# Kernel tuning notes

Measured on AMD Instinct MI355X. Metric: run time of the kernel, lower is better.

The kernel has to match this reference:

```python
import jax, jax.numpy as jnp
import numpy as np

THRESHOLD = 0.9  # graph_threshold; graph_secondary is None
EPS = 1e-12


def setup_inputs() -> dict:
    key = jax.random.key(0)
    k_x, k_cw, k_cb, k_u, k_lw, k_lb = jax.random.split(key, 6)
    B = 8192
    x = jax.random.normal(k_x, (B, 1, 28, 28), dtype=jnp.float32)
    conv_w = jax.random.normal(k_cw, (4, 1, 2, 2), dtype=jnp.float32) * 0.5  # OIHW
    conv_b = jax.random.normal(k_cb, (4,), dtype=jnp.float32) * 0.1
    # random orthogonal 4x4 "quantum" unitary via QR, as in the torch buffer
    unitary = jnp.linalg.qr(jax.random.normal(k_u, (4, 4), dtype=jnp.float32))[0]
    D = 4 * 14 * 14  # conv_out * num_patches = 784
    lin_w = jax.random.normal(k_lw, (10, D), dtype=jnp.float32) * (1.0 / np.sqrt(D))
    lin_b = jax.random.normal(k_lb, (10,), dtype=jnp.float32) * 0.01
    return {"x": x, "conv_w": conv_w, "conv_b": conv_b, "unitary": unitary,
            "lin_w": lin_w, "lin_b": lin_b}


def _forward(x, conv_w, conv_b, unitary, lin_w, lin_b):
    B = x.shape[0]
    # _PatchConv: 2x2 conv, stride 2, then flatten to [B, 4*14*14]
    feats = jax.lax.conv_general_dilated(
        x, conv_w, window_strides=(2, 2), padding="VALID",
        dimension_numbers=("NCHW", "OIHW", "NCHW"))
    feats = feats + conv_b[None, :, None, None]
    flat = feats.reshape(B, -1)                      # [B, 784]
    # _QuantumPatchEncoder: reinterpret as [B, 196, 4], apply unitary^T
    patches = flat.reshape(B, -1, 4)
    qf = jnp.einsum("bnk,wk->bnw", patches, unitary).reshape(B, -1)  # [B, 784]
    # linear head + log_softmax
    logits = qf @ lin_w.T + lin_b
    log_probs = jax.nn.log_softmax(logits, axis=-1)
    # GraphAdjacencyLayer: pairwise squared-cosine fidelity, thresholded.
    # Vectorized: normalize rows, one GEMM, square, threshold.
    qn = qf / (jnp.linalg.norm(qf, axis=-1, keepdims=True) + EPS)   # [B, 784]
    fid = (qn @ qn.T) ** 2                                          # [B, B]
    adj = jnp.where(fid >= THRESHOLD, 1.0, 0.0).astype(jnp.float32)
    adj = adj * (1.0 - jnp.eye(B, dtype=jnp.float32))  # no self-edges (i<j pairs)
    return log_probs, adj


def reference(x, conv_w, conv_b, unitary, lin_w, lin_b):
    return _forward(x, conv_w, conv_b, unitary, lin_w, lin_b)
```

## Files before the change

### kernel.cpp

```cpp
#include <hip/hip_runtime.h>
#include <hip/hip_bf16.h>

typedef unsigned char uchar_t;
typedef __attribute__((ext_vector_type(4))) float f32x4;

#define B_SZ 8192
#define D_FT 784
#define N_KT 13
#define PLANE_U32 131072
#define PLANE_B   524288
#define THRESH 0.9f

#define GLOBAL_AS(p) ((const __attribute__((address_space(1))) void*)(p))
#define LDS_AS(p)    ((__attribute__((address_space(3))) void*)(p))

__global__ __launch_bounds__(256) void preproc_kernel(
    const float* __restrict__ x, const float* __restrict__ conv_w,
    const float* __restrict__ conv_b, const float* __restrict__ unitary,
    const float* __restrict__ lin_w, const float* __restrict__ lin_b,
    float* __restrict__ log_probs, uchar_t* __restrict__ qn)
{
    __shared__ float xr[4][784];
    __shared__ float qf[4][784];

    const int t = threadIdx.x, lane = t & 63, wave = t >> 6;
    const int b = blockIdx.x * 4 + wave;
    float* xw = xr[wave];
    float* qw = qf[wave];

    const float4* xsrc = (const float4*)(x + (size_t)b * 784);
    #pragma unroll
    for (int i = lane; i < 196; i += 64) ((float4*)xw)[i] = xsrc[i];
    __syncthreads();

    float sumsq = 0.f;
    for (int g = lane; g < 196; g += 64) {
        const int c = g / 49, p = g % 49;
        const float w00 = conv_w[c*4+0], w01 = conv_w[c*4+1];
        const float w10 = conv_w[c*4+2], w11 = conv_w[c*4+3];
        const float bcv = conv_b[c];
        float feat[4];
        #pragma unroll
        for (int j = 0; j < 4; ++j) {
            const int s = 4*p + j;
            const int h = s / 14, wq = s % 14;
            const float* px = &xw[(2*h)*28 + 2*wq];
            feat[j] = bcv + w00*px[0] + w01*px[1] + w10*px[28] + w11*px[29];
        }
        #pragma unroll
        for (int w = 0; w < 4; ++w) {
            float v = unitary[w*4+0]*feat[0] + unitary[w*4+1]*feat[1]
                    + unitary[w*4+2]*feat[2] + unitary[w*4+3]*feat[3];
            qw[4*g + w] = v;
            sumsq += v * v;
        }
    }
    __syncthreads();

    #pragma unroll
    for (int off = 1; off < 64; off <<= 1) sumsq += __shfl_xor(sumsq, off, 64);
    const float inv = 1.0f / (sqrtf(sumsq) + 1e-12f);

    unsigned int* qbase = (unsigned int*)qn;
    for (int i = lane; i < 208; i += 64) {
        unsigned int o = 0u;
        if (i < 196) {
            const float v0 = qw[4*i+0] * inv, v1 = qw[4*i+1] * inv;
            const float v2 = qw[4*i+2] * inv, v3 = qw[4*i+3] * inv;
            int lo = __builtin_amdgcn_cvt_pk_fp8_f32(v0, v1, 0, 0);
            o = (unsigned int)__builtin_amdgcn_cvt_pk_fp8_f32(v2, v3, lo, 1);
        }
        qbase[(size_t)(i >> 4) * PLANE_U32 + (size_t)b * 16 + (i & 15)] = o;
    }

    float acc[10];
    #pragma unroll
    for (int cl = 0; cl < 10; ++cl) acc[cl] = 0.f;
    for (int k = lane; k < 784; k += 64) {
        const float v = qw[k];
        #pragma unroll
        for (int cl = 0; cl < 10; ++cl) acc[cl] += v * lin_w[cl*784 + k];
    }
    #pragma unroll
    for (int cl = 0; cl < 10; ++cl) {
        #pragma unroll
        for (int off = 1; off < 64; off <<= 1)
            acc[cl] += __shfl_xor(acc[cl], off, 64);
        acc[cl] += lin_b[cl];
    }
    if (lane == 0) {
        float mx = -1e30f;
        #pragma unroll
        for (int cl = 0; cl < 10; ++cl) mx = fmaxf(mx, acc[cl]);
        float se = 0.f;
        #pragma unroll
        for (int cl = 0; cl < 10; ++cl) se += expf(acc[cl] - mx);
        const float lse = mx + logf(se);
        #pragma unroll
        for (int cl = 0; cl < 10; ++cl)
            log_probs[(size_t)b*10 + cl] = acc[cl] - lse;
    }
}

__global__ __launch_bounds__(256, 4) void gram_kernel(
    const uchar_t* __restrict__ qn, float* __restrict__ adj)
{
    const int t0 = blockIdx.x;
    int tl = (t0 & 7) * 260 + (t0 >> 3);
    int br = (int)((129.0 - sqrt(16641.0 - 8.0 * (double)tl)) * 0.5);
    while ((br + 1) * (129 - (br + 1)) / 2 <= tl) ++br;
    while (br * (129 - br) / 2 > tl) --br;
    const int bc = br + (tl - br * (129 - br) / 2);

    __shared__ uchar_t ldsA[2][8192] __attribute__((aligned(16)));
    __shared__ uchar_t ldsB[2][8192] __attribute__((aligned(16)));

    const int t = threadIdx.x;
    const int lane = t & 63, wave = t >> 6;
    const int wr = wave >> 1, wc = wave & 1;
    const int quad = lane >> 4, l16 = lane & 15;

    const bool offdiag = (br != bc);
    const int br128 = br * 128, bc128 = bc * 128;
    const int zmask = offdiag ? 8191 : 4095;

    const int srow = lane & 15, sck = (lane >> 4) * 16;
    const uchar_t* gA0 = qn + (size_t)(br128 + wave*16     + srow) * 64 + sck;
    const uchar_t* gA1 = qn + (size_t)(br128 + (wave+4)*16 + srow) * 64 + sck;
    const uchar_t* gB0 = qn + (size_t)(bc128 + wave*16     + srow) * 64 + sck;
    const uchar_t* gB1 = qn + (size_t)(bc128 + (wave+4)*16 + srow) * 64 + sck;
    const int ld0 = wave * 1024, ld1 = (wave + 4) * 1024;

    #define STAGE(p, koff) do {                                                            \
        __builtin_amdgcn_global_load_lds(GLOBAL_AS(gA0 + (koff)), LDS_AS(&ldsA[p][ld0]), 16, 0, 0); \
        __builtin_amdgcn_global_load_lds(GLOBAL_AS(gA1 + (koff)), LDS_AS(&ldsA[p][ld1]), 16, 0, 0); \
        __builtin_amdgcn_global_load_lds(GLOBAL_AS(gB0 + (koff)), LDS_AS(&ldsB[p][ld0]), 16, 0, 0); \
        __builtin_amdgcn_global_load_lds(GLOBAL_AS(gB1 + (koff)), LDS_AS(&ldsB[p][ld1]), 16, 0, 0); \
    } while (0)

    f32x4 acc[4][4] = {};
    STAGE(0, 0);

    #pragma unroll
    for (int kt = 0; kt < N_KT; ++kt) {
        const int p = kt & 1;

        asm volatile("" ::: "memory");
        if (kt == 0)
            __builtin_amdgcn_s_waitcnt(0xF70);
        else
            __builtin_amdgcn_s_waitcnt(0xF73);
        __builtin_amdgcn_s_barrier();
        asm volatile("" ::: "memory");

        if (kt + 1 < N_KT) STAGE(p ^ 1, (size_t)(kt + 1) * PLANE_B);
        asm volatile("" ::: "memory");

        {
            f32x4 z = {0.f, 0.f, 0.f, 0.f};
            #pragma unroll
            for (int j = 0; j < 3; ++j) {
                const int idx  = (kt * 768 + j * 256 + t) & zmask;
                const int tile = idx >> 12;
                const int r    = (idx >> 5) & 127;
                const int c4   = idx & 31;
                const int rowb = tile ? bc128 : br128;
                const int colb = tile ? br128 : bc128;
                __builtin_nontemporal_store(
                    z, (f32x4*)adj + (size_t)(rowb + r) * 2048 + (colb >> 2) + c4);
            }
        }
        asm volatile("" ::: "memory");

        #pragma unroll
        for (int s = 0; s < 2; ++s) {
            const int fo = (2*s + (quad >> 1))*256 + l16*16 + (quad & 1)*8;
            long bfr[4];
            #pragma unroll
            for (int ni = 0; ni < 4; ++ni)
                bfr[ni] = *(const long*)&ldsB[p][(wc*4 + ni)*1024 + fo];
            #pragma unroll
            for (int mi = 0; mi < 4; ++mi) {
                const long af = *(const long*)&ldsA[p][(wr*4 + mi)*1024 + fo];
                #pragma unroll
                for (int ni = 0; ni < 4; ++ni)
                    acc[mi][ni] = __builtin_amdgcn_mfma_f32_16x16x32_fp8_fp8(
                        af, bfr[ni], acc[mi][ni], 0, 0, 0);
            }
        }
    }
    #undef STAGE

    asm volatile("" ::: "memory");
    __builtin_amdgcn_s_waitcnt(0xF70);
    __builtin_amdgcn_s_barrier();
    asm volatile("" ::: "memory");

    #pragma unroll
    for (int mi = 0; mi < 4; ++mi) {
        const int gr0 = br128 + wr*64 + mi*16 + quad*4;
        #pragma unroll
        for (int ni = 0; ni < 4; ++ni) {
            const int gc = bc128 + wc*64 + ni*16 + l16;
            const f32x4 v = acc[mi][ni];
            float o[4];
            bool h = false;
            #pragma unroll
            for (int r = 0; r < 4; ++r) {
                o[r] = (v[r]*v[r] >= THRESH && (gr0 + r) != gc) ? 1.0f : 0.0f;
                h = h || (o[r] != 0.0f);
            }
            if (__any(h)) {
                #pragma unroll
                for (int r = 0; r < 4; ++r)
                    adj[(size_t)(gr0 + r) * B_SZ + gc] = o[r];
                if (offdiag)
                    *(float4*)&adj[(size_t)gc * B_SZ + gr0] =
                        make_float4(o[0], o[1], o[2], o[3]);
            }
        }
    }
}

extern "C" void kernel_launch(void* const* d_in, const int* in_sizes, int n_in,
                              void* d_out, int out_size, void* d_ws, size_t ws_size,
                              hipStream_t stream) {
    const float* x       = (const float*)d_in[0];
    const float* conv_w  = (const float*)d_in[1];
    const float* conv_b  = (const float*)d_in[2];
    const float* unitary = (const float*)d_in[3];
    const float* lin_w   = (const float*)d_in[4];
    const float* lin_b   = (const float*)d_in[5];

    float* log_probs = (float*)d_out;
    float* adj       = (float*)d_out + (size_t)B_SZ * 10;
    uchar_t* qn      = (uchar_t*)d_ws;

    preproc_kernel<<<B_SZ / 4, 256, 0, stream>>>(x, conv_w, conv_b, unitary,
                                                 lin_w, lin_b, log_probs, qn);
    gram_kernel<<<2080, 256, 0, stream>>>(qn, adj);
}
```

Before: 340.4 us.

## Enlarge gram tiles to 256x256 with 32x32 MFMA and triple-buffered staging

Switches the symmetric gram kernel from 128x128 tiles with 16x16x32 fp8 MFMA to 256x256 tiles using 32x32x16 fp8 MFMA, with 512 threads per block. Operand staging moves from two to three LDS buffers, prefetching two k-steps ahead with adjusted waitcnt values. The zero-fill and threshold epilogue are rewritten for the new tile shape. This is meant to raise operand reuse and MFMA efficiency and to hide load latency, at the cost of far fewer blocks, possible tail imbalance, and higher LDS use that can limit occupancy.

```diff
diff --git a/kernel.cpp b/kernel.cpp
--- a/kernel.cpp
+++ b/kernel.cpp
@@ -2,7 +2,8 @@
 #include <hip/hip_bf16.h>
 
 typedef unsigned char uchar_t;
-typedef __attribute__((ext_vector_type(4))) float f32x4;
+typedef __attribute__((ext_vector_type(4)))  float f32x4;
+typedef __attribute__((ext_vector_type(16))) float f32x16;
 
 #define B_SZ 8192
 #define D_FT 784
@@ -102,34 +103,34 @@
     }
 }
 
-__global__ __launch_bounds__(256, 4) void gram_kernel(
+__global__ __launch_bounds__(512, 2) void gram_kernel(
     const uchar_t* __restrict__ qn, float* __restrict__ adj)
 {
     const int t0 = blockIdx.x;
-    int tl = (t0 & 7) * 260 + (t0 >> 3);
-    int br = (int)((129.0 - sqrt(16641.0 - 8.0 * (double)tl)) * 0.5);
-    while ((br + 1) * (129 - (br + 1)) / 2 <= tl) ++br;
-    while (br * (129 - br) / 2 > tl) --br;
-    const int bc = br + (tl - br * (129 - br) / 2);
-
-    __shared__ uchar_t ldsA[2][8192] __attribute__((aligned(16)));
-    __shared__ uchar_t ldsB[2][8192] __attribute__((aligned(16)));
+    int tl = (t0 & 7) * 66 + (t0 >> 3);
+    int br = (int)((65.0 - sqrt(4225.0 - 8.0 * (double)tl)) * 0.5);
+    while ((br + 1) * (65 - (br + 1)) / 2 <= tl) ++br;
+    while (br * (65 - br) / 2 > tl) --br;
+    const int bc = br + (tl - br * (65 - br) / 2);
+
+    __shared__ uchar_t ldsA[3][16384] __attribute__((aligned(16)));
+    __shared__ uchar_t ldsB[3][16384] __attribute__((aligned(16)));
 
     const int t = threadIdx.x;
     const int lane = t & 63, wave = t >> 6;
-    const int wr = wave >> 1, wc = wave & 1;
-    const int quad = lane >> 4, l16 = lane & 15;
+    const int wrow = wave >> 1, wcol = wave & 1;
+    const int l32 = lane & 31, half = lane >> 5;
 
     const bool offdiag = (br != bc);
-    const int br128 = br * 128, bc128 = bc * 128;
-    const int zmask = offdiag ? 8191 : 4095;
+    const int br256 = br * 256, bc256 = bc * 256;
+    const int zmask = offdiag ? 32767 : 16383;
 
     const int srow = lane & 15, sck = (lane >> 4) * 16;
-    const uchar_t* gA0 = qn + (size_t)(br128 + wave*16     + srow) * 64 + sck;
-    const uchar_t* gA1 = qn + (size_t)(br128 + (wave+4)*16 + srow) * 64 + sck;
-    const uchar_t* gB0 = qn + (size_t)(bc128 + wave*16     + srow) * 64 + sck;
-    const uchar_t* gB1 = qn + (size_t)(bc128 + (wave+4)*16 + srow) * 64 + sck;
-    const int ld0 = wave * 1024, ld1 = (wave + 4) * 1024;
+    const uchar_t* gA0 = qn + (size_t)(br256 + wave*16       + srow) * 64 + sck;
+    const uchar_t* gA1 = qn + (size_t)(br256 + (wave+8)*16   + srow) * 64 + sck;
+    const uchar_t* gB0 = qn + (size_t)(bc256 + wave*16       + srow) * 64 + sck;
+    const uchar_t* gB1 = qn + (size_t)(bc256 + (wave+8)*16   + srow) * 64 + sck;
+    const int ld0 = wave * 1024, ld1 = (wave + 8) * 1024;
 
     #define STAGE(p, koff) do {                                                            \
         __builtin_amdgcn_global_load_lds(GLOBAL_AS(gA0 + (koff)), LDS_AS(&ldsA[p][ld0]), 16, 0, 0); \
@@ -138,34 +139,47 @@
         __builtin_amdgcn_global_load_lds(GLOBAL_AS(gB1 + (koff)), LDS_AS(&ldsB[p][ld1]), 16, 0, 0); \
     } while (0)
 
-    f32x4 acc[4][4] = {};
+    int aoff[2], boff[4];
+    #pragma unroll
+    for (int mi = 0; mi < 2; ++mi) {
+        const int r = wrow*64 + mi*32 + l32;
+        aoff[mi] = (r >> 4)*1024 + (r & 15)*16 + half*8;
+    }
+    #pragma unroll
+    for (int ni = 0; ni < 4; ++ni) {
+        const int c = wcol*128 + ni*32 + l32;
+        boff[ni] = (c >> 4)*1024 + (c & 15)*16 + half*8;
+    }
+
+    f32x16 acc[2][4] = {};
     STAGE(0, 0);
+    STAGE(1, PLANE_B);
 
     #pragma unroll
     for (int kt = 0; kt < N_KT; ++kt) {
-        const int p = kt & 1;
-
-        asm volatile("" ::: "memory");
-        if (kt == 0)
-            __builtin_amdgcn_s_waitcnt(0xF70);
-        else
-            __builtin_amdgcn_s_waitcnt(0xF73);
+        const int p = kt % 3, p2 = (kt + 2) % 3;
+
+        asm volatile("" ::: "memory");
+        if (kt == 0)               __builtin_amdgcn_s_waitcnt(0xF74);
+        else if (kt == 1)          __builtin_amdgcn_s_waitcnt(0xF79);
+        else if (kt == N_KT - 1)   __builtin_amdgcn_s_waitcnt(0xF7A);
+        else                       __builtin_amdgcn_s_waitcnt(0xF7E);
         __builtin_amdgcn_s_barrier();
         asm volatile("" ::: "memory");
 
-        if (kt + 1 < N_KT) STAGE(p ^ 1, (size_t)(kt + 1) * PLANE_B);
+        if (kt + 2 < N_KT) STAGE(p2, (size_t)(kt + 2) * PLANE_B);
         asm volatile("" ::: "memory");
 
         {
             f32x4 z = {0.f, 0.f, 0.f, 0.f};
             #pragma unroll
-            for (int j = 0; j < 3; ++j) {
-                const int idx  = (kt * 768 + j * 256 + t) & zmask;
-                const int tile = idx >> 12;
-                const int r    = (idx >> 5) & 127;
-                const int c4   = idx & 31;
-                const int rowb = tile ? bc128 : br128;
-                const int colb = tile ? br128 : bc128;
+            for (int j = 0; j < 5; ++j) {
+                const int idx  = (kt * 2560 + j * 512 + t) & zmask;
+                const int tile = idx >> 14;
+                const int r    = (idx >> 6) & 255;
+                const int c4   = idx & 63;
+                const int rowb = tile ? bc256 : br256;
+                const int colb = tile ? br256 : bc256;
                 __builtin_nontemporal_store(
                     z, (f32x4*)adj + (size_t)(rowb + r) * 2048 + (colb >> 2) + c4);
             }
@@ -173,20 +187,21 @@
         asm volatile("" ::: "memory");
 
         #pragma unroll
-        for (int s = 0; s < 2; ++s) {
-            const int fo = (2*s + (quad >> 1))*256 + l16*16 + (quad & 1)*8;
-            long bfr[4];
-            #pragma unroll
-            for (int ni = 0; ni < 4; ++ni)
-                bfr[ni] = *(const long*)&ldsB[p][(wc*4 + ni)*1024 + fo];
-            #pragma unroll
-            for (int mi = 0; mi < 4; ++mi) {
-                const long af = *(const long*)&ldsA[p][(wr*4 + mi)*1024 + fo];
-                #pragma unroll
-                for (int ni = 0; ni < 4; ++ni)
-                    acc[mi][ni] = __builtin_amdgcn_mfma_f32_16x16x32_fp8_fp8(
-                        af, bfr[ni], acc[mi][ni], 0, 0, 0);
-            }
+        for (int s = 0; s < 4; ++s) {
+            long a0 = *(const long*)&ldsA[p][aoff[0] + s*256];
+            long a1 = *(const long*)&ldsA[p][aoff[1] + s*256];
+            long b0 = *(const long*)&ldsB[p][boff[0] + s*256];
+            long b1 = *(const long*)&ldsB[p][boff[1] + s*256];
+            long b2 = *(const long*)&ldsB[p][boff[2] + s*256];
+            long b3 = *(const long*)&ldsB[p][boff[3] + s*256];
+            acc[0][0] = __builtin_amdgcn_mfma_f32_32x32x16_fp8_fp8(a0, b0, acc[0][0], 0, 0, 0);
+            acc[1][0] = __builtin_amdgcn_mfma_f32_32x32x16_fp8_fp8(a1, b0, acc[1][0], 0, 0, 0);
+            acc[0][1] = __builtin_amdgcn_mfma_f32_32x32x16_fp8_fp8(a0, b1, acc[0][1], 0, 0, 0);
+            acc[1][1] = __builtin_amdgcn_mfma_f32_32x32x16_fp8_fp8(a1, b1, acc[1][1], 0, 0, 0);
+            acc[0][2] = __builtin_amdgcn_mfma_f32_32x32x16_fp8_fp8(a0, b2, acc[0][2], 0, 0, 0);
+            acc[1][2] = __builtin_amdgcn_mfma_f32_32x32x16_fp8_fp8(a1, b2, acc[1][2], 0, 0, 0);
+            acc[0][3] = __builtin_amdgcn_mfma_f32_32x32x16_fp8_fp8(a0, b3, acc[0][3], 0, 0, 0);
+            acc[1][3] = __builtin_amdgcn_mfma_f32_32x32x16_fp8_fp8(a1, b3, acc[1][3], 0, 0, 0);
         }
     }
     #undef STAGE
@@ -197,26 +212,31 @@
     asm volatile("" ::: "memory");
 
     #pragma unroll
-    for (int mi = 0; mi < 4; ++mi) {
-        const int gr0 = br128 + wr*64 + mi*16 + quad*4;
+    for (int mi = 0; mi < 2; ++mi) {
+        const int rbase = br256 + wrow*64 + mi*32 + 4*half;
         #pragma unroll
         for (int ni = 0; ni < 4; ++ni) {
-            const int gc = bc128 + wc*64 + ni*16 + l16;
-            const f32x4 v = acc[mi][ni];
-            float o[4];
-            bool h = false;
+            const int gc = bc256 + wcol*128 + ni*32 + l32;
+            const f32x16 v = acc[mi][ni];
             #pragma unroll
-            for (int r = 0; r < 4; ++r) {
-                o[r] = (v[r]*v[r] >= THRESH && (gr0 + r) != gc) ? 1.0f : 0.0f;
-                h = h || (o[r] != 0.0f);
-            }
-            if (__any(h)) {
+            for (int q = 0; q < 4; ++q) {
+                const int gr0 = rbase + 8*q;
+                float o[4];
+                bool h = false;
                 #pragma unroll
-                for (int r = 0; r < 4; ++r)
-                    adj[(size_t)(gr0 + r) * B_SZ + gc] = o[r];
-                if (offdiag)
-                    *(float4*)&adj[(size_t)gc * B_SZ + gr0] =
-                        make_float4(o[0], o[1], o[2], o[3]);
+                for (int r = 0; r < 4; ++r) {
+                    const float val = v[4*q + r];
+                    o[r] = (val*val >= THRESH && (gr0 + r) != gc) ? 1.0f : 0.0f;
+                    h = h || (o[r] != 0.0f);
+                }
+                if (__any(h)) {
+                    #pragma unroll
+                    for (int r = 0; r < 4; ++r)
+                        adj[(size_t)(gr0 + r) * B_SZ + gc] = o[r];
+                    if (offdiag)
+                        *(float4*)&adj[(size_t)gc * B_SZ + gr0] =
+                            make_float4(o[0], o[1], o[2], o[3]);
+                }
             }
         }
     }
@@ -238,5 +258,5 @@
 
     preproc_kernel<<<B_SZ / 4, 256, 0, stream>>>(x, conv_w, conv_b, unitary,
                                                  lin_w, lin_b, log_probs, qn);
-    gram_kernel<<<2080, 256, 0, stream>>>(qn, adj);
+    gram_kernel<<<528, 512, 0, stream>>>(qn, adj);
 }
```

Measured after the change: 346.4 us. About the same (+1.8%).

## Move adjacency zero-fill from gram loop into preprocessing kernel blocks

Applied to the files above, without the earlier changes.

Adds extra blocks to the first kernel that zero the whole adjacency matrix with a grid-stride loop, running alongside the per-sample preprocessing. The gram kernel no longer issues interleaved nontemporal zero stores inside its k-loop, so its waitcnt simplifies and the final barrier before the epilogue is dropped. This lightens the MFMA loop, but it gives up overlapping the large write stream with compute and now uses regular rather than nontemporal stores.

```diff
diff --git a/kernel.cpp b/kernel.cpp
--- a/kernel.cpp
+++ b/kernel.cpp
@@ -10,18 +10,31 @@
 #define PLANE_U32 131072
 #define PLANE_B   524288
 #define THRESH 0.9f
+#define PRE_BLKS 2048
+#define FILL_BLKS 4096
 
 #define GLOBAL_AS(p) ((const __attribute__((address_space(1))) void*)(p))
 #define LDS_AS(p)    ((__attribute__((address_space(3))) void*)(p))
 
-__global__ __launch_bounds__(256) void preproc_kernel(
+__global__ __launch_bounds__(256) void init_kernel(
     const float* __restrict__ x, const float* __restrict__ conv_w,
     const float* __restrict__ conv_b, const float* __restrict__ unitary,
     const float* __restrict__ lin_w, const float* __restrict__ lin_b,
-    float* __restrict__ log_probs, uchar_t* __restrict__ qn)
+    float* __restrict__ log_probs, uchar_t* __restrict__ qn,
+    float* __restrict__ adj)
 {
     __shared__ float xr[4][784];
     __shared__ float qf[4][784];
+
+    if (blockIdx.x >= PRE_BLKS) {
+        const size_t n4 = (size_t)B_SZ * B_SZ / 4;
+        f32x4 z = {0.f, 0.f, 0.f, 0.f};
+        f32x4* p = (f32x4*)adj;
+        for (size_t i = (size_t)(blockIdx.x - PRE_BLKS) * 256 + threadIdx.x;
+             i < n4; i += (size_t)FILL_BLKS * 256)
+            p[i] = z;
+        return;
+    }
 
     const int t = threadIdx.x, lane = t & 63, wave = t >> 6;
     const int b = blockIdx.x * 4 + wave;
@@ -122,7 +135,6 @@
 
     const bool offdiag = (br != bc);
     const int br128 = br * 128, bc128 = bc * 128;
-    const int zmask = offdiag ? 8191 : 4095;
 
     const int srow = lane & 15, sck = (lane >> 4) * 16;
     const uchar_t* gA0 = qn + (size_t)(br128 + wave*16     + srow) * 64 + sck;
@@ -146,30 +158,11 @@
         const int p = kt & 1;
 
         asm volatile("" ::: "memory");
-        if (kt == 0)
-            __builtin_amdgcn_s_waitcnt(0xF70);
-        else
-            __builtin_amdgcn_s_waitcnt(0xF73);
+        __builtin_amdgcn_s_waitcnt(0xF70);
         __builtin_amdgcn_s_barrier();
         asm volatile("" ::: "memory");
 
         if (kt + 1 < N_KT) STAGE(p ^ 1, (size_t)(kt + 1) * PLANE_B);
-        asm volatile("" ::: "memory");
-
-        {
-            f32x4 z = {0.f, 0.f, 0.f, 0.f};
-            #pragma unroll
-            for (int j = 0; j < 3; ++j) {
-                const int idx  = (kt * 768 + j * 256 + t) & zmask;
-                const int tile = idx >> 12;
-                const int r    = (idx >> 5) & 127;
-                const int c4   = idx & 31;
-                const int rowb = tile ? bc128 : br128;
-                const int colb = tile ? br128 : bc128;
-                __builtin_nontemporal_store(
-                    z, (f32x4*)adj + (size_t)(rowb + r) * 2048 + (colb >> 2) + c4);
-            }
-        }
         asm volatile("" ::: "memory");
 
         #pragma unroll
@@ -190,11 +183,6 @@
         }
     }
     #undef STAGE
-
-    asm volatile("" ::: "memory");
-    __builtin_amdgcn_s_waitcnt(0xF70);
-    __builtin_amdgcn_s_barrier();
-    asm volatile("" ::: "memory");
 
     #pragma unroll
     for (int mi = 0; mi < 4; ++mi) {
@@ -236,7 +224,7 @@
     float* adj       = (float*)d_out + (size_t)B_SZ * 10;
     uchar_t* qn      = (uchar_t*)d_ws;
 
-    preproc_kernel<<<B_SZ / 4, 256, 0, stream>>>(x, conv_w, conv_b, unitary,
-                                                 lin_w, lin_b, log_probs, qn);
+    init_kernel<<<PRE_BLKS + FILL_BLKS, 256, 0, stream>>>(
+        x, conv_w, conv_b, unitary, lin_w, lin_b, log_probs, qn, adj);
     gram_kernel<<<2080, 256, 0, stream>>>(qn, adj);
 }
```

Result: slower. 349.0 us (+2.5%).
